# Optimization experiments

Hardware: AMD Instinct MI355X
Metric: run time of the kernel (lower is better)

## Reference

```python
import jax, jax.numpy as jnp
import numpy as np


def setup_inputs() -> dict:
    key = jax.random.key(0)
    k1, k2, k3 = jax.random.split(key, 3)
    N, S = 65536, 128  # rays, samples per ray
    # t: sorted sample distances along each ray (near=2.0, far=6.0 typical NeRF bounds)
    t = jnp.sort(jax.random.uniform(k1, (N, S, 1), jnp.float32, 2.0, 6.0), axis=-2)
    # sigma: non-negative densities (post-ReLU/softplus output of NerfDensity)
    sigma = jax.random.uniform(k2, (N, S, 1), jnp.float32, 0.0, 2.0)
    # color: RGB in [0,1] (post-sigmoid output of NerfColor)
    color = jax.random.uniform(k3, (N, S, 3), jnp.float32, 0.0, 1.0)
    return {"t": t, "sigma": sigma, "color": color}


def integrate_ray(t, sigma, color, infinite=False):
    # t, sigma: [N, S, 1]; color: [N, S, 3]
    dt = t[..., 1:, :] - t[..., :-1, :]                      # [N, S-1, 1]
    last = 1e10 * jnp.ones_like(dt[..., 0:1, :]) if infinite else jnp.zeros_like(dt[..., 0:1, :])
    dt = jnp.concatenate((dt, last), axis=-2)                # [N, S, 1]
    sdt = sigma * dt                                         # [N, S, 1]
    Ti = jnp.exp(-jnp.cumsum(sdt, axis=-2))[..., 0:-1, :]    # transmittance, shifted
    Ti = jnp.concatenate((jnp.ones_like(Ti[..., 0:1, :]), Ti), axis=-2)
    alpha = 1.0 - jnp.exp(-sdt)
    wi = Ti * alpha                                          # [N, S, 1]
    return ((wi * color).sum(axis=-2), (wi * t).sum(axis=-2), wi, t)


def reference(t, sigma, color):
    # forward(): t is sorted along the sample dim before integration.
    t = jnp.sort(t, axis=-2)
    return integrate_ray(t, sigma, color, infinite=False)
```

## Files before the change

kernel.cpp:

```cpp
#include <hip/hip_runtime.h>
#include <math.h>


#define NRAYS 65536
#define S 128
#define RAYS_PER_BLOCK 8

typedef float __attribute__((ext_vector_type(4))) fvec4;

__global__ __launch_bounds__(256) void nerf_fused_kernel(
    const float* __restrict__ t,
    const float* __restrict__ sigma,
    const float* __restrict__ color,
    float* __restrict__ out_color,
    float* __restrict__ out_depth,
    float* __restrict__ out_wi,
    float* __restrict__ out_t)
{
    __shared__ fvec4 lds_c[RAYS_PER_BLOCK * S * 3 / 4];

    const int tid     = threadIdx.x;
    const int lane    = tid & 63;
    const int seglane = lane & 31;
    const int seg     = tid >> 5;
    const int ray     = blockIdx.x * RAYS_PER_BLOCK + seg;

    const long sbase = (long)ray * S + 4 * seglane;

    const fvec4* gc = (const fvec4*)(color + (long)blockIdx.x * (RAYS_PER_BLOCK * S * 3));
    const fvec4 g0 = __builtin_nontemporal_load(gc + tid);
    const fvec4 g1 = __builtin_nontemporal_load(gc + tid + 256);
    const fvec4 g2 = __builtin_nontemporal_load(gc + tid + 512);

    const fvec4 tv = __builtin_nontemporal_load((const fvec4*)(t + sbase));
    const fvec4 sv = __builtin_nontemporal_load((const fvec4*)(sigma + sbase));

    __builtin_nontemporal_store(tv, (fvec4*)(out_t + sbase));

    lds_c[tid]       = g0;
    lds_c[tid + 256] = g1;
    lds_c[tid + 512] = g2;
    __syncthreads();

    const int cidx = seg * (S * 3 / 4) + 3 * seglane;
    const fvec4 c0 = lds_c[cidx + 0];
    const fvec4 c1 = lds_c[cidx + 1];
    const fvec4 c2 = lds_c[cidx + 2];

    const float t_next = __shfl_down(tv.x, 1, 32);
    const float dt0 = tv.y - tv.x;
    const float dt1 = tv.z - tv.y;
    const float dt2 = tv.w - tv.z;
    const float dt3 = (seglane == 31) ? 0.0f : (t_next - tv.w);

    const float p0  = sv.x * dt0;
    const float p1  = p0 + sv.y * dt1;
    const float p2  = p1 + sv.z * dt2;
    const float tot = p2 + sv.w * dt3;

    float scan = tot;
    #pragma unroll
    for (int off = 1; off < 32; off <<= 1) {
        const float v = __shfl_up(scan, off, 32);
        if (seglane >= off) scan += v;
    }
    const float excl = scan - tot;

    const float E0 = __expf(-excl);
    const float e0 = __expf(-(excl + p0));
    const float e1 = __expf(-(excl + p1));
    const float e2 = __expf(-(excl + p2));
    const float e3 = __expf(-scan);
    const float wi0 = E0 - e0;
    const float wi1 = e0 - e1;
    const float wi2 = e1 - e2;
    const float wi3 = e2 - e3;

    fvec4 wiv; wiv.x = wi0; wiv.y = wi1; wiv.z = wi2; wiv.w = wi3;
    __builtin_nontemporal_store(wiv, (fvec4*)(out_wi + sbase));

    float r = wi0 * c0.x + wi1 * c0.w + wi2 * c1.z + wi3 * c2.y;
    float g = wi0 * c0.y + wi1 * c1.x + wi2 * c1.w + wi3 * c2.z;
    float b = wi0 * c0.z + wi1 * c1.y + wi2 * c2.x + wi3 * c2.w;
    float d = wi0 * tv.x + wi1 * tv.y + wi2 * tv.z + wi3 * tv.w;

    #pragma unroll
    for (int off = 16; off >= 1; off >>= 1) {
        r += __shfl_xor(r, off, 32);
        g += __shfl_xor(g, off, 32);
        b += __shfl_xor(b, off, 32);
        d += __shfl_xor(d, off, 32);
    }

    if (seglane == 0) {
        out_color[(long)ray * 3 + 0] = r;
        out_color[(long)ray * 3 + 1] = g;
        out_color[(long)ray * 3 + 2] = b;
        out_depth[ray] = d;
    }
}

extern "C" void kernel_launch(void* const* d_in, const int* in_sizes, int n_in,
                              void* d_out, int out_size, void* d_ws, size_t ws_size,
                              hipStream_t stream) {
    const float* t     = (const float*)d_in[0];
    const float* sigma = (const float*)d_in[1];
    const float* color = (const float*)d_in[2];

    float* out = (float*)d_out;
    float* out_color = out;
    float* out_depth = out_color + (long)NRAYS * 3;
    float* out_wi    = out_depth + NRAYS;
    float* out_t     = out_wi + (long)NRAYS * S;

    const int blocks = NRAYS / RAYS_PER_BLOCK;
    nerf_fused_kernel<<<blocks, 256, 0, stream>>>(
        t, sigma, color, out_color, out_depth, out_wi, out_t);
}
```

Baseline: 197.8 us.

## Process four tiles per block with register double-buffered prefetch and per-wave LDS

Each block now handles four 8-ray tiles in sequence and prefetches the next tile's t, sigma and color into registers while the current tile is computed. Each wave stages only its own two rays' colors in a private LDS slice, which removes the block-wide __syncthreads. The aim is to keep more loads in flight per wave and drop the barrier cost. In exchange the grid is four times smaller and each thread holds two sets of tile registers, which may lower occupancy.

```diff
diff --git a/kernel.cpp b/kernel.cpp
--- a/kernel.cpp
+++ b/kernel.cpp
@@ -4,59 +4,61 @@
 
 #define NRAYS 65536
 #define S 128
-#define RAYS_PER_BLOCK 8
+#define RAYS_PER_TILE 8
+#define TILES 4
+#define BLOCKS (NRAYS / (RAYS_PER_TILE * TILES))
 
 typedef float __attribute__((ext_vector_type(4))) fvec4;
 
-__global__ __launch_bounds__(256) void nerf_fused_kernel(
-    const float* __restrict__ t,
-    const float* __restrict__ sigma,
-    const float* __restrict__ color,
-    float* __restrict__ out_color,
-    float* __restrict__ out_depth,
-    float* __restrict__ out_wi,
-    float* __restrict__ out_t)
+struct TileRegs { fvec4 tv, sv, g0, g1, g2; };
+
+__device__ __forceinline__ TileRegs load_tile(
+    const float* __restrict__ t, const float* __restrict__ sigma,
+    const float* __restrict__ color, long tileIdx, int seg, int seglane,
+    int wave, int lane)
 {
-    __shared__ fvec4 lds_c[RAYS_PER_BLOCK * S * 3 / 4];
+    TileRegs r;
+    const long ray   = tileIdx * RAYS_PER_TILE + seg;
+    const long sbase = ray * S + 4 * seglane;
+    r.tv = __builtin_nontemporal_load((const fvec4*)(t + sbase));
+    r.sv = __builtin_nontemporal_load((const fvec4*)(sigma + sbase));
+    const fvec4* gc = (const fvec4*)(color +
+        (tileIdx * RAYS_PER_TILE + 2 * wave) * (long)(S * 3));
+    r.g0 = __builtin_nontemporal_load(gc + lane);
+    r.g1 = __builtin_nontemporal_load(gc + lane + 64);
+    r.g2 = __builtin_nontemporal_load(gc + lane + 128);
+    return r;
+}
 
-    const int tid     = threadIdx.x;
-    const int lane    = tid & 63;
-    const int seglane = lane & 31;
-    const int seg     = tid >> 5;
-    const int ray     = blockIdx.x * RAYS_PER_BLOCK + seg;
+__device__ __forceinline__ void compute_tile(
+    const TileRegs& R, fvec4* __restrict__ lds_w, long tileIdx, int seg,
+    int seglane, int lane,
+    float* __restrict__ out_color, float* __restrict__ out_depth,
+    float* __restrict__ out_wi, float* __restrict__ out_t)
+{
+    const long ray   = tileIdx * RAYS_PER_TILE + seg;
+    const long sbase = ray * S + 4 * seglane;
 
-    const long sbase = (long)ray * S + 4 * seglane;
+    __builtin_nontemporal_store(R.tv, (fvec4*)(out_t + sbase));
 
-    const fvec4* gc = (const fvec4*)(color + (long)blockIdx.x * (RAYS_PER_BLOCK * S * 3));
-    const fvec4 g0 = __builtin_nontemporal_load(gc + tid);
-    const fvec4 g1 = __builtin_nontemporal_load(gc + tid + 256);
-    const fvec4 g2 = __builtin_nontemporal_load(gc + tid + 512);
+    lds_w[lane]       = R.g0;
+    lds_w[lane + 64]  = R.g1;
+    lds_w[lane + 128] = R.g2;
+    const int cidx = (lane >> 5) * 96 + 3 * seglane;
+    const fvec4 c0 = lds_w[cidx + 0];
+    const fvec4 c1 = lds_w[cidx + 1];
+    const fvec4 c2 = lds_w[cidx + 2];
 
-    const fvec4 tv = __builtin_nontemporal_load((const fvec4*)(t + sbase));
-    const fvec4 sv = __builtin_nontemporal_load((const fvec4*)(sigma + sbase));
+    const float t_next = __shfl_down(R.tv.x, 1, 32);
+    const float dt0 = R.tv.y - R.tv.x;
+    const float dt1 = R.tv.z - R.tv.y;
+    const float dt2 = R.tv.w - R.tv.z;
+    const float dt3 = (seglane == 31) ? 0.0f : (t_next - R.tv.w);
 
-    __builtin_nontemporal_store(tv, (fvec4*)(out_t + sbase));
-
-    lds_c[tid]       = g0;
-    lds_c[tid + 256] = g1;
-    lds_c[tid + 512] = g2;
-    __syncthreads();
-
-    const int cidx = seg * (S * 3 / 4) + 3 * seglane;
-    const fvec4 c0 = lds_c[cidx + 0];
-    const fvec4 c1 = lds_c[cidx + 1];
-    const fvec4 c2 = lds_c[cidx + 2];
-
-    const float t_next = __shfl_down(tv.x, 1, 32);
-    const float dt0 = tv.y - tv.x;
-    const float dt1 = tv.z - tv.y;
-    const float dt2 = tv.w - tv.z;
-    const float dt3 = (seglane == 31) ? 0.0f : (t_next - tv.w);
-
-    const float p0  = sv.x * dt0;
-    const float p1  = p0 + sv.y * dt1;
-    const float p2  = p1 + sv.z * dt2;
-    const float tot = p2 + sv.w * dt3;
+    const float p0  = R.sv.x * dt0;
+    const float p1  = p0 + R.sv.y * dt1;
+    const float p2  = p1 + R.sv.z * dt2;
+    const float tot = p2 + R.sv.w * dt3;
 
     float scan = tot;
     #pragma unroll
@@ -82,7 +84,7 @@
     float r = wi0 * c0.x + wi1 * c0.w + wi2 * c1.z + wi3 * c2.y;
     float g = wi0 * c0.y + wi1 * c1.x + wi2 * c1.w + wi3 * c2.z;
     float b = wi0 * c0.z + wi1 * c1.y + wi2 * c2.x + wi3 * c2.w;
-    float d = wi0 * tv.x + wi1 * tv.y + wi2 * tv.z + wi3 * tv.w;
+    float d = wi0 * R.tv.x + wi1 * R.tv.y + wi2 * R.tv.z + wi3 * R.tv.w;
 
     #pragma unroll
     for (int off = 16; off >= 1; off >>= 1) {
@@ -93,10 +95,42 @@
     }
 
     if (seglane == 0) {
-        out_color[(long)ray * 3 + 0] = r;
-        out_color[(long)ray * 3 + 1] = g;
-        out_color[(long)ray * 3 + 2] = b;
+        out_color[ray * 3 + 0] = r;
+        out_color[ray * 3 + 1] = g;
+        out_color[ray * 3 + 2] = b;
         out_depth[ray] = d;
+    }
+}
+
+__global__ __launch_bounds__(256) void nerf_fused_kernel(
+    const float* __restrict__ t,
+    const float* __restrict__ sigma,
+    const float* __restrict__ color,
+    float* __restrict__ out_color,
+    float* __restrict__ out_depth,
+    float* __restrict__ out_wi,
+    float* __restrict__ out_t)
+{
+    __shared__ fvec4 lds_c[4][192];
+
+    const int tid     = threadIdx.x;
+    const int lane    = tid & 63;
+    const int seglane = tid & 31;
+    const int wave    = tid >> 6;
+    const int seg     = tid >> 5;
+
+    fvec4* lds_w = lds_c[wave];
+    const long base = (long)blockIdx.x * TILES;
+
+    TileRegs cur = load_tile(t, sigma, color, base, seg, seglane, wave, lane);
+    #pragma unroll
+    for (int r = 0; r < TILES; ++r) {
+        TileRegs nxt;
+        if (r + 1 < TILES)
+            nxt = load_tile(t, sigma, color, base + r + 1, seg, seglane, wave, lane);
+        compute_tile(cur, lds_w, base + r, seg, seglane, lane,
+                     out_color, out_depth, out_wi, out_t);
+        cur = nxt;
     }
 }
 
@@ -113,7 +147,6 @@
     float* out_wi    = out_depth + NRAYS;
     float* out_t     = out_wi + (long)NRAYS * S;
 
-    const int blocks = NRAYS / RAYS_PER_BLOCK;
-    nerf_fused_kernel<<<blocks, 256, 0, stream>>>(
+    nerf_fused_kernel<<<BLOCKS, 256, 0, stream>>>(
         t, sigma, color, out_color, out_depth, out_wi, out_t);
 }
```

New measurement: 203.2 us. 1.03x slower.
